# Kernel tuning notes

Hardware: AMD Instinct MI355X
Metric: run time of the kernel (lower is better)

## Reference

```python
import jax, jax.numpy as jnp
import numpy as np

T, B, E, H = 1024, 4, 1024, 16
Dh = E // H
NEG_INF = float('-inf')


def setup_inputs() -> dict:
    key = jax.random.key(0)
    k1, k2, k3, k4 = jax.random.split(key, 4)
    return {
        'fwd_x': jax.random.normal(k1, (T, B, E), jnp.float32),
        'bwd_x': jax.random.normal(k2, (T, B, E), jnp.float32),
        'in_proj_weight': jax.random.normal(k3, (3 * E, E), jnp.float32) * 0.02,
        'in_proj_bias': jnp.zeros((3 * E,), jnp.float32),
        'out_w': jax.random.normal(k4, (E, E), jnp.float32) * 0.02,
        'out_b': jnp.zeros((E,), jnp.float32),
    }


def reference(fwd_x, bwd_x, in_proj_weight, in_proj_bias, out_w, out_b):
    t, b, e = fwd_x.shape
    s = 2 * t
    dtype = fwd_x.dtype
    zeros = jnp.zeros((1, b, e), dtype)
    # padded_fwd_x[0:t] -> [0, fwd_x[:-1]]; padded_bwd_x[1:t+1] -> [bwd_x[1:], 0]
    q_in = jnp.concatenate([zeros, fwd_x[:-1]], 0) + jnp.concatenate([bwd_x[1:], zeros], 0)
    kv = jnp.concatenate([fwd_x, bwd_x], 0)  # [s, b, e]

    wq, wk, wv = in_proj_weight[:e], in_proj_weight[e:2 * e], in_proj_weight[2 * e:]
    bq, bk, bv = in_proj_bias[:e], in_proj_bias[e:2 * e], in_proj_bias[2 * e:]
    q = (q_in @ wq.T + bq).reshape(t, b, H, Dh)
    k = (kv @ wk.T + bk).reshape(s, b, H, Dh)
    v = (kv @ wv.T + bv).reshape(s, b, H, Dh)

    # NOTE: original module never applies self.scaling in forward -- keep unscaled.
    attn_weights = jnp.einsum('tbhd,sbhd->bhts', q, k)  # [b, H, t, s]

    # mask_curr_state=True: allowed keys are j < i (fwd half) or j > i + t (bwd half)
    i = jnp.arange(t)[:, None]
    j = jnp.arange(s)[None, :]
    allowed = (j >= i + t + 1) | (j <= i - 1)
    mask_bias = jnp.where(allowed, 0.0, NEG_INF).astype(dtype)
    attn_weights = attn_weights + mask_bias[None, None]

    probs = jax.nn.softmax(attn_weights.astype(jnp.float32), axis=-1).astype(dtype)

    attn = jnp.einsum('bhts,sbhd->tbhd', probs, v).reshape(t, b, e)
    attn = attn @ out_w.T + out_b
    avg_weights = probs.mean(axis=1)  # [b, t, s]
    return attn, avg_weights
```

## Files before the change

### kernel.cpp

```cpp
#include <hip/hip_runtime.h>

typedef unsigned short u16;
typedef __attribute__((ext_vector_type(8))) short short8;
typedef __attribute__((ext_vector_type(4))) float f32x4;

#define SM_SHIFT2 34.6246800f
#if defined(__has_builtin)
#if __has_builtin(__builtin_amdgcn_exp2f)
#define EXP2(x) __builtin_amdgcn_exp2f(x)
#else
#define EXP2(x) __expf((x) * 0.6931471805599453f)
#endif
#else
#define EXP2(x) __expf((x) * 0.6931471805599453f)
#endif

__device__ __forceinline__ u16 f2b(float f) {
  unsigned u = __float_as_uint(f);
  unsigned r = (u + 0x7FFFu + ((u >> 16) & 1u)) >> 16;
  return (u16)r;
}

__device__ __forceinline__ void gload16(const u16* g, u16* l) {
  __builtin_amdgcn_global_load_lds((const __attribute__((address_space(1))) void*)g,
                                   (__attribute__((address_space(3))) void*)l, 16, 0, 0);
}

__device__ __forceinline__ void cast4(const float* __restrict__ src,
                                      u16* __restrict__ dst, int gid) {
  float4 v = *(const float4*)(src + (gid << 2));
  ushort4 o; o.x = f2b(v.x); o.y = f2b(v.y); o.z = f2b(v.z); o.w = f2b(v.w);
  *(ushort4*)(dst + (gid << 2)) = o;
}

__global__ __launch_bounds__(256) void prep_all(const float* __restrict__ fwd,
                                                const float* __restrict__ bwd,
                                                const float* __restrict__ w_in,
                                                const float* __restrict__ w_out,
                                                u16* __restrict__ qin,
                                                u16* __restrict__ kvf,
                                                u16* __restrict__ kvb,
                                                u16* __restrict__ wbf,
                                                u16* __restrict__ wobf,
                                                float* __restrict__ out_avg) {
  const int blk = blockIdx.x, tid = threadIdx.x;
  if (blk < 4096) {
    int gid = blk * 256 + tid;
    int n = gid >> 8;
    int e4 = (gid & 255) << 2;
    int t = n >> 2, b = n & 3;
    float4 acc = make_float4(0.f, 0.f, 0.f, 0.f);
    if (t > 0) {
      float4 v = *(const float4*)(fwd + (((t - 1) * 4 + b) << 10) + e4);
      acc.x += v.x; acc.y += v.y; acc.z += v.z; acc.w += v.w;
    }
    if (t < 1023) {
      float4 v = *(const float4*)(bwd + (((t + 1) * 4 + b) << 10) + e4);
      acc.x += v.x; acc.y += v.y; acc.z += v.z; acc.w += v.w;
    }
    ushort4 o; o.x = f2b(acc.x); o.y = f2b(acc.y); o.z = f2b(acc.z); o.w = f2b(acc.w);
    *(ushort4*)(qin + (n << 10) + e4) = o;
  } else if (blk < 8192) {
    cast4(fwd, kvf, (blk - 4096) * 256 + tid);
  } else if (blk < 12288) {
    cast4(bwd, kvb, (blk - 8192) * 256 + tid);
  } else if (blk < 15360) {
    cast4(w_in, wbf, (blk - 12288) * 256 + tid);
  } else if (blk < 16384) {
    cast4(w_out, wobf, (blk - 15360) * 256 + tid);
  } else {
    int z = blk - 16384;
    int mi = z % 15, bt2 = z / 15;
    int tb2 = bt2 & 15, b2 = bt2 >> 4;
    int s0z = (tb2 + 1 + mi) << 6, t0z = tb2 << 6;
    float* ob = out_avg + (size_t)b2 * 2097152 + (size_t)t0z * 2048 + s0z;
    float4 zz = make_float4(0.f, 0.f, 0.f, 0.f);
#pragma unroll
    for (int it = 0; it < 4; ++it) {
      int idx = it * 256 + tid;
      int rr = idx >> 4, c4 = (idx & 15) << 2;
      *(float4*)&ob[rr * 2048 + c4] = zz;
    }
  }
}

__global__ __launch_bounds__(512, 2) void gemm_kv256(const u16* __restrict__ A,
                                                     const u16* __restrict__ W,
                                                     const float* __restrict__ bias,
                                                     u16* __restrict__ outK,
                                                     u16* __restrict__ outVt) {
  __shared__ u16 SH[65536];
  const int x = blockIdx.x & 7, local = blockIdx.x >> 3;
  const int mt = x * 4 + (local & 3);
  const int nt = local >> 2;
  const int m0 = mt << 8, n0 = nt << 8;
  const int tid = threadIdx.x;
  const int lane = tid & 63, wid = tid >> 6;
  const int wm = (wid >> 2) << 7;
  const int wn = (wid & 3) << 6;
  const int lr = lane & 15, lg = lane >> 4;
  const int co0 = ((lg ^ (lr & 7)) << 3);
  const int co1 = (((4 + lg) ^ (lr & 7)) << 3);
  const int rl = tid >> 3, ch = tid & 7;
  const int ssw = ((ch ^ (rl & 7)) << 3);
  const int arow = (rl & 31) + ((rl >> 5) << 7);
  f32x4 acc[8][4] = {};
  auto At = [&](int buf) { return SH + buf * 16384; };
  auto Wt = [&](int buf) { return SH + 32768 + buf * 16384; };
  auto stage_w2 = [&](int buf, int k0, int h) {
    int wr0 = (h << 7) + rl;
    gload16(&W[(size_t)(n0 + wr0) * 1024 + k0 + ssw], &Wt(buf)[wr0 * 64 + ch * 8]);
    int wr1 = wr0 + 64;
    gload16(&W[(size_t)(n0 + wr1) * 1024 + k0 + ssw], &Wt(buf)[wr1 * 64 + ch * 8]);
  };
  auto stage_a2 = [&](int buf, int k0, int h) {
    int ar0 = (h << 6) + arow;
    gload16(&A[(size_t)(m0 + ar0) * 1024 + k0 + ssw], &At(buf)[ar0 * 64 + ch * 8]);
    int ar1 = ar0 + 32;
    gload16(&A[(size_t)(m0 + ar1) * 1024 + k0 + ssw], &At(buf)[ar1 * 64 + ch * 8]);
  };
  stage_w2(0, 0, 0); stage_w2(0, 0, 1); stage_a2(0, 0, 0); stage_a2(0, 0, 1);
  short8 wf[4][2];
  for (int t = 0; t < 16; ++t) {
    const int cur = t & 1;
    const u16* a = At(cur);
    const u16* w = Wt(cur);
    const bool pf = (t < 15);
    const int nk0 = (t + 1) << 6;
#pragma unroll
    for (int q = 0; q < 4; ++q) {
      if (q == 0)      asm volatile("s_waitcnt vmcnt(3)" ::: "memory");
      else if (q == 1) { if (pf) asm volatile("s_waitcnt vmcnt(4)" ::: "memory");
                         else    asm volatile("s_waitcnt vmcnt(2)" ::: "memory"); }
      else if (q == 2) { if (pf) asm volatile("s_waitcnt vmcnt(5)" ::: "memory");
                         else    asm volatile("s_waitcnt vmcnt(1)" ::: "memory"); }
      else             { if (pf) asm volatile("s_waitcnt vmcnt(6)" ::: "memory");
                         else    asm volatile("s_waitcnt vmcnt(0)" ::: "memory"); }
      __builtin_amdgcn_s_barrier();
      if (pf) {
        if (q == 0) stage_w2(cur ^ 1, nk0, 0);
        else if (q == 1) stage_w2(cur ^ 1, nk0, 1);
        else if (q == 2) stage_a2(cur ^ 1, nk0, 0);
        else stage_a2(cur ^ 1, nk0, 1);
      }
      if (q == 0) {
#pragma unroll
        for (int j = 0; j < 4; ++j) {
          int wrow = (wn + j * 16 + lr) * 64;
          wf[j][0] = *(const short8*)&w[wrow + co0];
          wf[j][1] = *(const short8*)&w[wrow + co1];
        }
      }
      short8 af[2][2];
#pragma unroll
      for (int di = 0; di < 2; ++di) {
        int row = (wm + (2 * q + di) * 16 + lr) * 64;
        af[di][0] = *(const short8*)&a[row + co0];
        af[di][1] = *(const short8*)&a[row + co1];
      }
      __builtin_amdgcn_s_setprio(1);
#pragma unroll
      for (int dk = 0; dk < 2; ++dk)
#pragma unroll
        for (int di = 0; di < 2; ++di)
#pragma unroll
          for (int j = 0; j < 4; ++j)
            acc[2 * q + di][j] =
                __builtin_amdgcn_mfma_f32_16x16x32_bf16(af[di][dk], wf[j][dk],
                                                        acc[2 * q + di][j], 0, 0, 0);
      __builtin_amdgcn_s_setprio(0);
    }
  }
  __syncthreads();
  u16* C = SH;
  const bool isK = (n0 < 1024);
  if (isK) {
#pragma unroll
    for (int i = 0; i < 8; i++) {
#pragma unroll
      for (int j = 0; j < 4; j++) {
        int n = wn + j * 16 + lr;
        float bv = bias[n0 + n];
        int np = n ^ (lg << 4);
#pragma unroll
        for (int r = 0; r < 4; r++) {
          int m = wm + i * 16 + lg * 4 + r;
          C[m * 256 + np] = f2b(acc[i][j][r] + bv);
        }
      }
    }
    __syncthreads();
    const int hbase = n0 >> 6;
    const int ts0 = m0 >> 2;
    const int ts = tid >> 3, c8d = tid & 7;
#pragma unroll
    for (int k = 0; k < 16; ++k) {
      int tb = k >> 2, hh = k & 3;
      int m = ts * 4 + tb;
      int c8 = (hh * 8 + c8d) ^ ((ts & 3) << 1);
      uint4 val = *(const uint4*)&C[m * 256 + c8 * 8];
      size_t off = ((size_t)(tb * 16 + hbase + hh) * 2048 + ts0 + ts) * 64 + c8d * 8;
      *(uint4*)&outK[off] = val;
    }
  } else {
#pragma unroll
    for (int i = 0; i < 8; i++) {
#pragma unroll
      for (int j = 0; j < 4; j++) {
        int n = wn + j * 16 + lr;
        float bv = bias[n0 + n];
        int key = ((n & 7) ^ ((n >> 3) & 7)) << 3;
#pragma unroll
        for (int r = 0; r < 4; r++) {
          int u = (wm >> 2) + i * 4 + lg + (r << 6);
          C[n * 256 + (u ^ key)] = f2b(acc[i][j][r] + bv);
        }
      }
    }
    __syncthreads();
    const int dg0 = n0 - 1024;
    const int ts0 = m0 >> 2;
    const int nn = tid >> 3, tsg = tid & 7;
#pragma unroll
    for (int k = 0; k < 16; ++k) {
      int tb = k >> 2, nc = k & 3;
      int n = nc * 64 + nn;
      int key = ((n & 7) ^ ((n >> 3) & 7)) << 3;
      int chunk = ((tb << 6) + tsg * 8) ^ key;
      uint4 val = *(const uint4*)&C[n * 256 + chunk];
      int d = dg0 + n, h = d >> 6, dl = d & 63;
      size_t off = ((size_t)((tb * 16 + h) * 64 + dl)) * 2048 + ts0 + tsg * 8;
      *(uint4*)&outVt[off] = val;
    }
  }
}

template <int MODE, int MTX>
__global__ __launch_bounds__(256) void gemm_bt(const u16* __restrict__ A,
                                               const u16* __restrict__ W,
                                               const float* __restrict__ bias,
                                               void* __restrict__ outp) {
  __shared__ u16 At[2][128 * 64];
  __shared__ u16 Wt[2][128 * 64];
  const int x = blockIdx.x & 7, local = blockIdx.x >> 3;
  const int mt = x * MTX + (local % MTX);
  const int nt = local / MTX;
  const int m0 = mt << 7, n0 = nt << 7;
  const int tid = threadIdx.x;
  const int lane = tid & 63, wid = tid >> 6;
  const int wm = (wid >> 1) << 6, wn = (wid & 1) << 6;
  const int lr = lane & 15, lg = lane >> 4;
  const int srow = lane >> 3, scol = (lane & 7) << 3;
  const int swc = ((lane & 7) ^ srow) << 3;
  f32x4 acc[4][4] = {};
  auto stage = [&](int buf, int k0) {
#pragma unroll
    for (int it = 0; it < 4; it++) {
      int row = (it * 4 + wid) * 8 + srow;
      gload16(&A[(m0 + row) * 1024 + k0 + swc], &At[buf][row * 64 + scol]);
      gload16(&W[(n0 + row) * 1024 + k0 + swc], &Wt[buf][row * 64 + scol]);
    }
  };
  auto compute = [&](int buf) {
#pragma unroll
    for (int kk = 0; kk < 64; kk += 32) {
      short8 af[4], bf[4];
#pragma unroll
      for (int i = 0; i < 4; i++) {
        int co = (((kk >> 3) + lg) ^ (lr & 7)) << 3;
        af[i] = *(const short8*)&At[buf][(wm + i * 16 + lr) * 64 + co];
        bf[i] = *(const short8*)&Wt[buf][(wn + i * 16 + lr) * 64 + co];
      }
#pragma unroll
      for (int i = 0; i < 4; i++)
#pragma unroll
        for (int j = 0; j < 4; j++)
          acc[i][j] = __builtin_amdgcn_mfma_f32_16x16x32_bf16(af[i], bf[j], acc[i][j], 0, 0, 0);
    }
  };
  stage(0, 0);
  __syncthreads();
  for (int step = 0; step < 16; ++step) {
    const int cur = step & 1;
    if (step < 15) stage(cur ^ 1, (step + 1) << 6);
    compute(cur);
    __syncthreads();
  }
#pragma unroll
  for (int i = 0; i < 4; i++) {
#pragma unroll
    for (int j = 0; j < 4; j++) {
      int n = n0 + wn + j * 16 + lr;
      float bv = bias[n];
#pragma unroll
      for (int r = 0; r < 4; r++) {
        int m = m0 + wm + i * 16 + lg * 4 + r;
        float v = acc[i][j][r] + bv;
        if (MODE == 3) {
          ((float*)outp)[m * 1024 + n] = v;
        } else {
          v *= 1.44269504f;
          int tb = m & 3, ts = m >> 2, hh = n >> 6, d = n & 63;
          ((u16*)outp)[((tb * 16 + hh) * 1024 + ts) * 64 + d] = f2b(v);
        }
      }
    }
  }
}

__global__ __launch_bounds__(256) void attn_fwd(const u16* __restrict__ qb,
                                                const u16* __restrict__ kb,
                                                const u16* __restrict__ vtb,
                                                u16* __restrict__ attn_bf,
                                                float* __restrict__ st_il) {
  __shared__ u16 Kt[64 * 64];
  __shared__ u16 Vt[64 * 64];
  __shared__ u16 Pt[4][16 * 72];
  const int g = blockIdx.x;
  const int L = ((g & 7) << 7) | (g >> 3);
  const int t0 = (L & 15) << 6;
  const int h = (L >> 4) & 15;
  const int b = L >> 8;
  const int tid = threadIdx.x, lane = tid & 63, w = tid >> 6;
  const int lr = lane & 15, lg = lane >> 4;
  const int bh = b * 16 + h;
  const int sw0 = ((lg ^ (lr & 7)) << 3);
  const int sw1 = sw0 ^ 32;
  const u16* qrow = qb + ((bh << 10) + t0 + (w << 4) + lr) * 64;
  short8 qf0 = *(const short8*)&qrow[lg * 8];
  short8 qf1 = *(const short8*)&qrow[32 + lg * 8];
  const u16* kbase = kb + (size_t)(bh << 11) * 64;
  const u16* vbase = vtb + (size_t)(bh << 6) * 2048;
  f32x4 acc[4] = {};
  f32x4 accl = {};
  const int n1 = (t0 >> 6) + 1;
  const int grow = lane >> 3, gcol = (lane & 7) << 3;
  short8 ones;
#pragma unroll
  for (int j = 0; j < 8; ++j) ones[j] = (short)0x3F80;
  for (int ti = 0; ti < 17; ++ti) {
    const int s0 = (ti < n1) ? (ti << 6) : (t0 + 1024 + ((ti - n1) << 6));
    __syncthreads();
#pragma unroll
    for (int it = 0; it < 2; ++it) {
      int row = (it * 4 + w) * 8 + grow;
      int swc = (((lane & 7) ^ (row & 7)) << 3);
      gload16(&kbase[(size_t)(s0 + row) * 64 + swc], &Kt[row * 64 + gcol]);
      gload16(&vbase[(size_t)row * 2048 + s0 + swc], &Vt[row * 64 + gcol]);
    }
    __syncthreads();
    float pv[4][4];
    const bool maskt = (ti == n1 - 1) || (ti == n1);
    if (maskt) {
#pragma unroll
      for (int c = 0; c < 4; c++) {
        f32x4 sc = {};
        short8 kf0 = *(const short8*)&Kt[(c * 16 + lr) * 64 + sw0];
        short8 kf1 = *(const short8*)&Kt[(c * 16 + lr) * 64 + sw1];
        sc = __builtin_amdgcn_mfma_f32_16x16x32_bf16(qf0, kf0, sc, 0, 0, 0);
        sc = __builtin_amdgcn_mfma_f32_16x16x32_bf16(qf1, kf1, sc, 0, 0, 0);
        int j = s0 + c * 16 + lr;
#pragma unroll
        for (int r = 0; r < 4; r++) {
          int i = t0 + (w << 4) + lg * 4 + r;
          float e = EXP2(sc[r] - SM_SHIFT2);
          pv[c][r] = ((j < i) || (j > i + 1024)) ? e : 0.f;
        }
      }
    } else {
#pragma unroll
      for (int c = 0; c < 4; c++) {
        f32x4 sc = {};
        short8 kf0 = *(const short8*)&Kt[(c * 16 + lr) * 64 + sw0];
        short8 kf1 = *(const short8*)&Kt[(c * 16 + lr) * 64 + sw1];
        sc = __builtin_amdgcn_mfma_f32_16x16x32_bf16(qf0, kf0, sc, 0, 0, 0);
        sc = __builtin_amdgcn_mfma_f32_16x16x32_bf16(qf1, kf1, sc, 0, 0, 0);
#pragma unroll
        for (int r = 0; r < 4; r++)
          pv[c][r] = EXP2(sc[r] - SM_SHIFT2);
      }
    }
#pragma unroll
    for (int c = 0; c < 4; c++)
#pragma unroll
      for (int r = 0; r < 4; r++)
        Pt[w][(lg * 4 + r) * 72 + c * 16 + lr] = f2b(pv[c][r]);
    short8 pf0 = *(const short8*)&Pt[w][lr * 72 + lg * 8];
    short8 pf1 = *(const short8*)&Pt[w][lr * 72 + 32 + lg * 8];
    accl = __builtin_amdgcn_mfma_f32_16x16x32_bf16(pf0, ones, accl, 0, 0, 0);
    accl = __builtin_amdgcn_mfma_f32_16x16x32_bf16(pf1, ones, accl, 0, 0, 0);
#pragma unroll
    for (int dd = 0; dd < 4; dd++) {
      short8 vf0 = *(const short8*)&Vt[(dd * 16 + lr) * 64 + sw0];
      short8 vf1 = *(const short8*)&Vt[(dd * 16 + lr) * 64 + sw1];
      acc[dd] = __builtin_amdgcn_mfma_f32_16x16x32_bf16(pf0, vf0, acc[dd], 0, 0, 0);
      acc[dd] = __builtin_amdgcn_mfma_f32_16x16x32_bf16(pf1, vf1, acc[dd], 0, 0, 0);
    }
  }
  float inv[4];
#pragma unroll
  for (int r = 0; r < 4; r++) inv[r] = 1.f / accl[r];
  const int trow = t0 + (w << 4) + lg * 4;
#pragma unroll
  for (int dd = 0; dd < 4; dd++)
#pragma unroll
    for (int r = 0; r < 4; r++)
      attn_bf[((trow + r) * 4 + b) * 1024 + h * 64 + dd * 16 + lr] = f2b(acc[dd][r] * inv[r]);
#pragma unroll
  for (int r = 0; r < 4; r++)
    if (lr == r)
      st_il[(bh << 10) + trow + r] = inv[r];
}

__global__ __launch_bounds__(256) void attn_avg(const u16* __restrict__ qb,
                                                const u16* __restrict__ kb,
                                                const float* __restrict__ st_il,
                                                float* __restrict__ avg) {
  __shared__ u16 Kt[2][64 * 64];
  __shared__ float Si[16][64];
  const int g = blockIdx.x;
  const int L = (g & 7) * 136 + (g >> 3);
  const int l = L % 17;
  const int bt = L / 17;
  const int tb = bt & 15, b = bt >> 4;
  const int sb = (l <= tb) ? l : l + 15;
  const int s0 = sb << 6, t0 = tb << 6;
  const bool maskblk = (l == tb) || (l == tb + 1);
  const int tid = threadIdx.x, lane = tid & 63, w = tid >> 6;
  const int lr = lane & 15, lg = lane >> 4;
  const int trow = t0 + (w << 4) + lg * 4;
  float* obase = avg + (size_t)b * 2097152;
  for (int i = tid; i < 1024; i += 256) {
    int hh = i >> 6, tt = i & 63;
    Si[hh][tt] = st_il[(((b << 4) + hh) << 10) + t0 + tt];
  }
  const int sw0 = ((lg ^ (lr & 7)) << 3);
  const int sw1 = sw0 ^ 32;
  const int grow = lane >> 3, gcol = (lane & 7) << 3;
  const int srr = (w << 4) + lg * 4;
  auto stage = [&](int buf, int hh) {
    const u16* kb_h = kb + ((size_t)(((b << 4) + hh) << 11) + s0) * 64;
#pragma unroll
    for (int it = 0; it < 2; ++it) {
      int row = it * 32 + w * 8 + grow;
      int swc = (((lane & 7) ^ grow) << 3);
      gload16(&kb_h[(size_t)row * 64 + swc], &Kt[buf][row * 64 + gcol]);
    }
  };
  stage(0, 0);
  __syncthreads();
  float accv[4][4] = {};
  for (int h = 0; h < 16; h++) {
    const int cur = h & 1;
    if (h < 15) stage(cur ^ 1, h + 1);
    const int bh = (b << 4) + h;
    const u16* qrow = qb + ((bh << 10) + t0 + (w << 4) + lr) * 64;
    short8 qf0 = *(const short8*)&qrow[lg * 8];
    short8 qf1 = *(const short8*)&qrow[32 + lg * 8];
    float ih[4];
#pragma unroll
    for (int r = 0; r < 4; r++) ih[r] = Si[h][srr + r];
    if (maskblk) {
#pragma unroll
      for (int c = 0; c < 4; c++) {
        f32x4 sc = {};
        short8 kf0 = *(const short8*)&Kt[cur][(c * 16 + lr) * 64 + sw0];
        short8 kf1 = *(const short8*)&Kt[cur][(c * 16 + lr) * 64 + sw1];
        sc = __builtin_amdgcn_mfma_f32_16x16x32_bf16(qf0, kf0, sc, 0, 0, 0);
        sc = __builtin_amdgcn_mfma_f32_16x16x32_bf16(qf1, kf1, sc, 0, 0, 0);
        int j = s0 + c * 16 + lr;
#pragma unroll
        for (int r = 0; r < 4; r++) {
          int i = t0 + (w << 4) + lg * 4 + r;
          if ((j < i) || (j > i + 1024))
            accv[c][r] += EXP2(sc[r] - SM_SHIFT2) * ih[r];
        }
      }
    } else {
#pragma unroll
      for (int c = 0; c < 4; c++) {
        f32x4 sc = {};
        short8 kf0 = *(const short8*)&Kt[cur][(c * 16 + lr) * 64 + sw0];
        short8 kf1 = *(const short8*)&Kt[cur][(c * 16 + lr) * 64 + sw1];
        sc = __builtin_amdgcn_mfma_f32_16x16x32_bf16(qf0, kf0, sc, 0, 0, 0);
        sc = __builtin_amdgcn_mfma_f32_16x16x32_bf16(qf1, kf1, sc, 0, 0, 0);
#pragma unroll
        for (int r = 0; r < 4; r++)
          accv[c][r] += EXP2(sc[r] - SM_SHIFT2) * ih[r];
      }
    }
    __syncthreads();
  }
#pragma unroll
  for (int c = 0; c < 4; c++)
#pragma unroll
    for (int r = 0; r < 4; r++)
      obase[(trow + r) * 2048 + s0 + c * 16 + lr] = accv[c][r] * 0.0625f;
}

extern "C" void kernel_launch(void* const* d_in, const int* in_sizes, int n_in,
                              void* d_out, int out_size, void* d_ws, size_t ws_size,
                              hipStream_t stream) {
  const float* fwd   = (const float*)d_in[0];
  const float* bwd   = (const float*)d_in[1];
  const float* w_in  = (const float*)d_in[2];
  const float* b_in  = (const float*)d_in[3];
  const float* w_out = (const float*)d_in[4];
  const float* b_out = (const float*)d_in[5];

  char* ws = (char*)d_ws;
  u16*  q_in_bf = (u16*)(ws);
  u16*  kv_bf   = (u16*)(ws + 8388608);
  u16*  w_bf    = (u16*)(ws + 25165824);
  u16*  wo_bf   = (u16*)(ws + 31457280);
  u16*  q_bf    = (u16*)(ws + 33554432);
  u16*  k_bf    = (u16*)(ws + 41943040);
  u16*  vt_bf   = (u16*)(ws + 58720256);
  u16*  attn_bf = (u16*)(ws + 75497472);
  float* st_il  = (float*)(ws + 83886080);

  float* out_attn = (float*)d_out;
  float* out_avg  = (float*)d_out + 4194304;

  prep_all<<<17344, 256, 0, stream>>>(fwd, bwd, w_in, w_out, q_in_bf, kv_bf,
                                      kv_bf + 4194304, w_bf, wo_bf, out_avg);

  gemm_bt<0, 4><<<256, 256, 0, stream>>>(q_in_bf, w_bf, b_in, (void*)q_bf);
  gemm_kv256<<<256, 512, 0, stream>>>(kv_bf, w_bf + 1048576, b_in + 1024,
                                      k_bf, vt_bf);

  attn_fwd<<<1024, 256, 0, stream>>>(q_bf, k_bf, vt_bf, attn_bf, st_il);

  gemm_bt<3, 4><<<256, 256, 0, stream>>>(attn_bf, wo_bf, b_out,
                                         (void*)out_attn);

  attn_avg<<<1088, 256, 0, stream>>>(q_bf, k_bf, st_il, out_avg);
}
```

Before: 168.2 us.

## Merge Q projection into KV GEMM launch and fuse output GEMM with avg kernel

The Q projection now runs as 64 extra 256x256 tiles inside the KV projection kernel, with the log2e scale folded into its epilogue, so the standalone 128-tile Q GEMM launch goes away. The output projection GEMM and the attention-average kernel become one launch that dispatches on block index, letting the two independent tail stages share the GPU. This removes two launches and their tail gaps. In exchange, the fused out-projection path drops double buffering and syncs twice per k-step, and blocks of mixed shape may balance poorly.

Result: slower. 172.5 us (+2.5%).

```diff
diff --git a/kernel.cpp b/kernel.cpp
--- a/kernel.cpp
+++ b/kernel.cpp
@@ -84,16 +84,33 @@
   }
 }
 
-__global__ __launch_bounds__(512, 2) void gemm_kv256(const u16* __restrict__ A,
-                                                     const u16* __restrict__ W,
-                                                     const float* __restrict__ bias,
-                                                     u16* __restrict__ outK,
-                                                     u16* __restrict__ outVt) {
+__global__ __launch_bounds__(512, 2) void proj_qkv(const u16* __restrict__ kvA,
+                                                   const u16* __restrict__ Wkv,
+                                                   const float* __restrict__ bkv,
+                                                   const u16* __restrict__ qA,
+                                                   const u16* __restrict__ Wq,
+                                                   const float* __restrict__ bq,
+                                                   u16* __restrict__ outK,
+                                                   u16* __restrict__ outVt,
+                                                   u16* __restrict__ outQ) {
   __shared__ u16 SH[65536];
-  const int x = blockIdx.x & 7, local = blockIdx.x >> 3;
-  const int mt = x * 4 + (local & 3);
-  const int nt = local >> 2;
-  const int m0 = mt << 8, n0 = nt << 8;
+  const int bid = blockIdx.x;
+  const u16* A; const u16* W; const float* bias;
+  int m0, n0, path;
+  if (bid < 256) {
+    const int x = bid & 7, local = bid >> 3;
+    m0 = (x * 4 + (local & 3)) << 8;
+    n0 = (local >> 2) << 8;
+    A = kvA; W = Wkv; bias = bkv;
+    path = (n0 < 1024) ? 0 : 1;
+  } else {
+    const int l2 = bid - 256;
+    const int x = l2 & 7, loc = l2 >> 3;
+    m0 = ((x << 1) + (loc & 1)) << 8;
+    n0 = (loc >> 1) << 8;
+    A = qA; W = Wq; bias = bq;
+    path = 2;
+  }
   const int tid = threadIdx.x;
   const int lane = tid & 63, wid = tid >> 6;
   const int wm = (wid >> 2) << 7;
@@ -173,36 +190,7 @@
   }
   __syncthreads();
   u16* C = SH;
-  const bool isK = (n0 < 1024);
-  if (isK) {
-#pragma unroll
-    for (int i = 0; i < 8; i++) {
-#pragma unroll
-      for (int j = 0; j < 4; j++) {
-        int n = wn + j * 16 + lr;
-        float bv = bias[n0 + n];
-        int np = n ^ (lg << 4);
-#pragma unroll
-        for (int r = 0; r < 4; r++) {
-          int m = wm + i * 16 + lg * 4 + r;
-          C[m * 256 + np] = f2b(acc[i][j][r] + bv);
-        }
-      }
-    }
-    __syncthreads();
-    const int hbase = n0 >> 6;
-    const int ts0 = m0 >> 2;
-    const int ts = tid >> 3, c8d = tid & 7;
-#pragma unroll
-    for (int k = 0; k < 16; ++k) {
-      int tb = k >> 2, hh = k & 3;
-      int m = ts * 4 + tb;
-      int c8 = (hh * 8 + c8d) ^ ((ts & 3) << 1);
-      uint4 val = *(const uint4*)&C[m * 256 + c8 * 8];
-      size_t off = ((size_t)(tb * 16 + hbase + hh) * 2048 + ts0 + ts) * 64 + c8d * 8;
-      *(uint4*)&outK[off] = val;
-    }
-  } else {
+  if (path == 1) {
 #pragma unroll
     for (int i = 0; i < 8; i++) {
 #pragma unroll
@@ -232,78 +220,36 @@
       size_t off = ((size_t)((tb * 16 + h) * 64 + dl)) * 2048 + ts0 + tsg * 8;
       *(uint4*)&outVt[off] = val;
     }
-  }
-}
-
-template <int MODE, int MTX>
-__global__ __launch_bounds__(256) void gemm_bt(const u16* __restrict__ A,
-                                               const u16* __restrict__ W,
-                                               const float* __restrict__ bias,
-                                               void* __restrict__ outp) {
-  __shared__ u16 At[2][128 * 64];
-  __shared__ u16 Wt[2][128 * 64];
-  const int x = blockIdx.x & 7, local = blockIdx.x >> 3;
-  const int mt = x * MTX + (local % MTX);
-  const int nt = local / MTX;
-  const int m0 = mt << 7, n0 = nt << 7;
-  const int tid = threadIdx.x;
-  const int lane = tid & 63, wid = tid >> 6;
-  const int wm = (wid >> 1) << 6, wn = (wid & 1) << 6;
-  const int lr = lane & 15, lg = lane >> 4;
-  const int srow = lane >> 3, scol = (lane & 7) << 3;
-  const int swc = ((lane & 7) ^ srow) << 3;
-  f32x4 acc[4][4] = {};
-  auto stage = [&](int buf, int k0) {
-#pragma unroll
-    for (int it = 0; it < 4; it++) {
-      int row = (it * 4 + wid) * 8 + srow;
-      gload16(&A[(m0 + row) * 1024 + k0 + swc], &At[buf][row * 64 + scol]);
-      gload16(&W[(n0 + row) * 1024 + k0 + swc], &Wt[buf][row * 64 + scol]);
-    }
-  };
-  auto compute = [&](int buf) {
-#pragma unroll
-    for (int kk = 0; kk < 64; kk += 32) {
-      short8 af[4], bf[4];
-#pragma unroll
-      for (int i = 0; i < 4; i++) {
-        int co = (((kk >> 3) + lg) ^ (lr & 7)) << 3;
-        af[i] = *(const short8*)&At[buf][(wm + i * 16 + lr) * 64 + co];
-        bf[i] = *(const short8*)&Wt[buf][(wn + i * 16 + lr) * 64 + co];
-      }
-#pragma unroll
-      for (int i = 0; i < 4; i++)
-#pragma unroll
-        for (int j = 0; j < 4; j++)
-          acc[i][j] = __builtin_amdgcn_mfma_f32_16x16x32_bf16(af[i], bf[j], acc[i][j], 0, 0, 0);
-    }
-  };
-  stage(0, 0);
-  __syncthreads();
-  for (int step = 0; step < 16; ++step) {
-    const int cur = step & 1;
-    if (step < 15) stage(cur ^ 1, (step + 1) << 6);
-    compute(cur);
+  } else {
+    const float scl = (path == 2) ? 1.44269504f : 1.0f;
+#pragma unroll
+    for (int i = 0; i < 8; i++) {
+#pragma unroll
+      for (int j = 0; j < 4; j++) {
+        int n = wn + j * 16 + lr;
+        float bv = bias[n0 + n];
+        int np = n ^ (lg << 4);
+#pragma unroll
+        for (int r = 0; r < 4; r++) {
+          int m = wm + i * 16 + lg * 4 + r;
+          C[m * 256 + np] = f2b((acc[i][j][r] + bv) * scl);
+        }
+      }
+    }
     __syncthreads();
-  }
-#pragma unroll
-  for (int i = 0; i < 4; i++) {
-#pragma unroll
-    for (int j = 0; j < 4; j++) {
-      int n = n0 + wn + j * 16 + lr;
-      float bv = bias[n];
-#pragma unroll
-      for (int r = 0; r < 4; r++) {
-        int m = m0 + wm + i * 16 + lg * 4 + r;
-        float v = acc[i][j][r] + bv;
-        if (MODE == 3) {
-          ((float*)outp)[m * 1024 + n] = v;
-        } else {
-          v *= 1.44269504f;
-          int tb = m & 3, ts = m >> 2, hh = n >> 6, d = n & 63;
-          ((u16*)outp)[((tb * 16 + hh) * 1024 + ts) * 64 + d] = f2b(v);
-        }
-      }
+    u16* ob = (path == 0) ? outK : outQ;
+    const int SS = (path == 0) ? 2048 : 1024;
+    const int hbase = n0 >> 6;
+    const int ts0 = m0 >> 2;
+    const int ts = tid >> 3, c8d = tid & 7;
+#pragma unroll
+    for (int k = 0; k < 16; ++k) {
+      int tb = k >> 2, hh = k & 3;
+      int m = ts * 4 + tb;
+      int c8 = (hh * 8 + c8d) ^ ((ts & 3) << 1);
+      uint4 val = *(const uint4*)&C[m * 256 + c8 * 8];
+      size_t off = ((size_t)(tb * 16 + hbase + hh) * SS + ts0 + ts) * 64 + c8d * 8;
+      *(uint4*)&ob[off] = val;
     }
   }
 }
@@ -412,90 +358,149 @@
       st_il[(bh << 10) + trow + r] = inv[r];
 }
 
-__global__ __launch_bounds__(256) void attn_avg(const u16* __restrict__ qb,
-                                                const u16* __restrict__ kb,
-                                                const float* __restrict__ st_il,
-                                                float* __restrict__ avg) {
-  __shared__ u16 Kt[2][64 * 64];
-  __shared__ float Si[16][64];
-  const int g = blockIdx.x;
-  const int L = (g & 7) * 136 + (g >> 3);
-  const int l = L % 17;
-  const int bt = L / 17;
-  const int tb = bt & 15, b = bt >> 4;
-  const int sb = (l <= tb) ? l : l + 15;
-  const int s0 = sb << 6, t0 = tb << 6;
-  const bool maskblk = (l == tb) || (l == tb + 1);
-  const int tid = threadIdx.x, lane = tid & 63, w = tid >> 6;
+__global__ __launch_bounds__(256) void tail_mega(const u16* __restrict__ qb,
+                                                 const u16* __restrict__ kb,
+                                                 const float* __restrict__ st_il,
+                                                 float* __restrict__ avg,
+                                                 const u16* __restrict__ attA,
+                                                 const u16* __restrict__ wo,
+                                                 const float* __restrict__ bo,
+                                                 float* __restrict__ out_attn) {
+  __shared__ __align__(16) u16 SM[16384];
+  const int bid = blockIdx.x, tid = threadIdx.x;
+  const int lane = tid & 63, w = tid >> 6;
   const int lr = lane & 15, lg = lane >> 4;
-  const int trow = t0 + (w << 4) + lg * 4;
-  float* obase = avg + (size_t)b * 2097152;
-  for (int i = tid; i < 1024; i += 256) {
-    int hh = i >> 6, tt = i & 63;
-    Si[hh][tt] = st_il[(((b << 4) + hh) << 10) + t0 + tt];
+  if (bid < 1088) {
+    u16* KtF = SM;
+    float* Si = (float*)(SM + 8192);
+    const int L = (bid & 7) * 136 + (bid >> 3);
+    const int l = L % 17;
+    const int bt = L / 17;
+    const int tb = bt & 15, b = bt >> 4;
+    const int sb = (l <= tb) ? l : l + 15;
+    const int s0 = sb << 6, t0 = tb << 6;
+    const bool maskblk = (l == tb) || (l == tb + 1);
+    const int trow = t0 + (w << 4) + lg * 4;
+    float* obase = avg + (size_t)b * 2097152;
+    for (int i = tid; i < 1024; i += 256) {
+      int hh = i >> 6, tt = i & 63;
+      Si[hh * 64 + tt] = st_il[(((b << 4) + hh) << 10) + t0 + tt];
+    }
+    const int sw0 = ((lg ^ (lr & 7)) << 3);
+    const int sw1 = sw0 ^ 32;
+    const int grow = lane >> 3, gcol = (lane & 7) << 3;
+    const int srr = (w << 4) + lg * 4;
+    auto stage = [&](int buf, int hh) {
+      const u16* kb_h = kb + ((size_t)(((b << 4) + hh) << 11) + s0) * 64;
+#pragma unroll
+      for (int it = 0; it < 2; ++it) {
+        int row = it * 32 + w * 8 + grow;
+        int swc = (((lane & 7) ^ grow) << 3);
+        gload16(&kb_h[(size_t)row * 64 + swc], &KtF[buf * 4096 + row * 64 + gcol]);
+      }
+    };
+    stage(0, 0);
+    __syncthreads();
+    float accv[4][4] = {};
+    for (int h = 0; h < 16; h++) {
+      const int cur = h & 1;
+      if (h < 15) stage(cur ^ 1, h + 1);
+      const int bh = (b << 4) + h;
+      const u16* qrow = qb + ((bh << 10) + t0 + (w << 4) + lr) * 64;
+      short8 qf0 = *(const short8*)&qrow[lg * 8];
+      short8 qf1 = *(const short8*)&qrow[32 + lg * 8];
+      float ih[4];
+#pragma unroll
+      for (int r = 0; r < 4; r++) ih[r] = Si[h * 64 + srr + r];
+      const u16* Kc = KtF + cur * 4096;
+      if (maskblk) {
+#pragma unroll
+        for (int c = 0; c < 4; c++) {
+          f32x4 sc = {};
+          short8 kf0 = *(const short8*)&Kc[(c * 16 + lr) * 64 + sw0];
+          short8 kf1 = *(const short8*)&Kc[(c * 16 + lr) * 64 + sw1];
+          sc = __builtin_amdgcn_mfma_f32_16x16x32_bf16(qf0, kf0, sc, 0, 0, 0);
+          sc = __builtin_amdgcn_mfma_f32_16x16x32_bf16(qf1, kf1, sc, 0, 0, 0);
+          int j = s0 + c * 16 + lr;
+#pragma unroll
+          for (int r = 0; r < 4; r++) {
+            int i = t0 + (w << 4) + lg * 4 + r;
+            if ((j < i) || (j > i + 1024))
+              accv[c][r] += EXP2(sc[r] - SM_SHIFT2) * ih[r];
+          }
+        }
+      } else {
+#pragma unroll
+        for (int c = 0; c < 4; c++) {
+          f32x4 sc = {};
+          short8 kf0 = *(const short8*)&Kc[(c * 16 + lr) * 64 + sw0];
+          short8 kf1 = *(const short8*)&Kc[(c * 16 + lr) * 64 + sw1];
+          sc = __builtin_amdgcn_mfma_f32_16x16x32_bf16(qf0, kf0, sc, 0, 0, 0);
+          sc = __builtin_amdgcn_mfma_f32_16x16x32_bf16(qf1, kf1, sc, 0, 0, 0);
+#pragma unroll
+          for (int r = 0; r < 4; r++)
+            accv[c][r] += EXP2(sc[r] - SM_SHIFT2) * ih[r];
+        }
+      }
+      __syncthreads();
+    }
+#pragma unroll
+    for (int c = 0; c < 4; c++)
+#pragma unroll
+      for (int r = 0; r < 4; r++)
+        obase[(trow + r) * 2048 + s0 + c * 16 + lr] = accv[c][r] * 0.0625f;
+  } else {
+    u16* At = SM;
+    u16* Wt = SM + 8192;
+    const int b2 = bid - 1088;
+    const int x = b2 & 7, local = b2 >> 3;
+    const int mt = x * 4 + (local & 3);
+    const int nt = local >> 2;
+    const int m0 = mt << 7, n0 = nt << 7;
+    const int wid = w;
+    const int wm = (wid >> 1) << 6, wn = (wid & 1) << 6;
+    const int srow = lane >> 3, scol = (lane & 7) << 3;
+    const int swc = ((lane & 7) ^ srow) << 3;
+    f32x4 acc[4][4] = {};
+    for (int step = 0; step < 16; ++step) {
+      __syncthreads();
+#pragma unroll
+      for (int it = 0; it < 4; it++) {
+        int row = (it * 4 + wid) * 8 + srow;
+        gload16(&attA[(m0 + row) * 1024 + (step << 6) + swc], &At[row * 64 + scol]);
+        gload16(&wo[(n0 + row) * 1024 + (step << 6) + swc], &Wt[row * 64 + scol]);
+      }
+      __syncthreads();
+#pragma unroll
+      for (int kk = 0; kk < 64; kk += 32) {
+        short8 af[4], bf[4];
+#pragma unroll
+        for (int i = 0; i < 4; i++) {
+          int co = (((kk >> 3) + lg) ^ (lr & 7)) << 3;
+          af[i] = *(const short8*)&At[(wm + i * 16 + lr) * 64 + co];
+          bf[i] = *(const short8*)&Wt[(wn + i * 16 + lr) * 64 + co];
+        }
+#pragma unroll
+        for (int i = 0; i < 4; i++)
+#pragma unroll
+          for (int j = 0; j < 4; j++)
+            acc[i][j] = __builtin_amdgcn_mfma_f32_16x16x32_bf16(af[i], bf[j], acc[i][j], 0, 0, 0);
+      }
+    }
+#pragma unroll
+    for (int i = 0; i < 4; i++) {
+#pragma unroll
+      for (int j = 0; j < 4; j++) {
+        int n = n0 + wn + j * 16 + lr;
+        float bv = bo[n];
+#pragma unroll
+        for (int r = 0; r < 4; r++) {
+          int m = m0 + wm + i * 16 + lg * 4 + r;
+          out_attn[m * 1024 + n] = acc[i][j][r] + bv;
+        }
+      }
+    }
   }
-  const int sw0 = ((lg ^ (lr & 7)) << 3);
-  const int sw1 = sw0 ^ 32;
-  const int grow = lane >> 3, gcol = (lane & 7) << 3;
-  const int srr = (w << 4) + lg * 4;
-  auto stage = [&](int buf, int hh) {
-    const u16* kb_h = kb + ((size_t)(((b << 4) + hh) << 11) + s0) * 64;
-#pragma unroll
-    for (int it = 0; it < 2; ++it) {
-      int row = it * 32 + w * 8 + grow;
-      int swc = (((lane & 7) ^ grow) << 3);
-      gload16(&kb_h[(size_t)row * 64 + swc], &Kt[buf][row * 64 + gcol]);
-    }
-  };
-  stage(0, 0);
-  __syncthreads();
-  float accv[4][4] = {};
-  for (int h = 0; h < 16; h++) {
-    const int cur = h & 1;
-    if (h < 15) stage(cur ^ 1, h + 1);
-    const int bh = (b << 4) + h;
-    const u16* qrow = qb + ((bh << 10) + t0 + (w << 4) + lr) * 64;
-    short8 qf0 = *(const short8*)&qrow[lg * 8];
-    short8 qf1 = *(const short8*)&qrow[32 + lg * 8];
-    float ih[4];
-#pragma unroll
-    for (int r = 0; r < 4; r++) ih[r] = Si[h][srr + r];
-    if (maskblk) {
-#pragma unroll
-      for (int c = 0; c < 4; c++) {
-        f32x4 sc = {};
-        short8 kf0 = *(const short8*)&Kt[cur][(c * 16 + lr) * 64 + sw0];
-        short8 kf1 = *(const short8*)&Kt[cur][(c * 16 + lr) * 64 + sw1];
-        sc = __builtin_amdgcn_mfma_f32_16x16x32_bf16(qf0, kf0, sc, 0, 0, 0);
-        sc = __builtin_amdgcn_mfma_f32_16x16x32_bf16(qf1, kf1, sc, 0, 0, 0);
-        int j = s0 + c * 16 + lr;
-#pragma unroll
-        for (int r = 0; r < 4; r++) {
-          int i = t0 + (w << 4) + lg * 4 + r;
-          if ((j < i) || (j > i + 1024))
-            accv[c][r] += EXP2(sc[r] - SM_SHIFT2) * ih[r];
-        }
-      }
-    } else {
-#pragma unroll
-      for (int c = 0; c < 4; c++) {
-        f32x4 sc = {};
-        short8 kf0 = *(const short8*)&Kt[cur][(c * 16 + lr) * 64 + sw0];
-        short8 kf1 = *(const short8*)&Kt[cur][(c * 16 + lr) * 64 + sw1];
-        sc = __builtin_amdgcn_mfma_f32_16x16x32_bf16(qf0, kf0, sc, 0, 0, 0);
-        sc = __builtin_amdgcn_mfma_f32_16x16x32_bf16(qf1, kf1, sc, 0, 0, 0);
-#pragma unroll
-        for (int r = 0; r < 4; r++)
-          accv[c][r] += EXP2(sc[r] - SM_SHIFT2) * ih[r];
-      }
-    }
-    __syncthreads();
-  }
-#pragma unroll
-  for (int c = 0; c < 4; c++)
-#pragma unroll
-    for (int r = 0; r < 4; r++)
-      obase[(trow + r) * 2048 + s0 + c * 16 + lr] = accv[c][r] * 0.0625f;
 }
 
 extern "C" void kernel_launch(void* const* d_in, const int* in_sizes, int n_in,
@@ -525,14 +530,12 @@
   prep_all<<<17344, 256, 0, stream>>>(fwd, bwd, w_in, w_out, q_in_bf, kv_bf,
                                       kv_bf + 4194304, w_bf, wo_bf, out_avg);
 
-  gemm_bt<0, 4><<<256, 256, 0, stream>>>(q_in_bf, w_bf, b_in, (void*)q_bf);
-  gemm_kv256<<<256, 512, 0, stream>>>(kv_bf, w_bf + 1048576, b_in + 1024,
-                                      k_bf, vt_bf);
+  proj_qkv<<<320, 512, 0, stream>>>(kv_bf, w_bf + 1048576, b_in + 1024,
+                                    q_in_bf, w_bf, b_in,
+                                    k_bf, vt_bf, q_bf);
 
   attn_fwd<<<1024, 256, 0, stream>>>(q_bf, k_bf, vt_bf, attn_bf, st_il);
 
-  gemm_bt<3, 4><<<256, 256, 0, stream>>>(attn_bf, wo_bf, b_out,
-                                         (void*)out_attn);
-
-  attn_avg<<<1088, 256, 0, stream>>>(q_bf, k_bf, st_il, out_avg);
-}
+  tail_mega<<<1344, 256, 0, stream>>>(q_bf, k_bf, st_il, out_avg,
+                                      attn_bf, wo_bf, b_out, out_attn);
+}
```

## Fuse output projection GEMM and attention-average kernel into one launch

Applied to the files above, without the earlier changes.

Merges the output-projection GEMM and the head-averaged probability kernel into a single heterogeneous kernel. Block IDs are split into groups of 21: 17 blocks compute avg-weights tiles and 4 compute 128x128 GEMM tiles, so the two independent workloads run concurrently and share the GPU. This removes one launch and the tail/serialization gap between the two kernels. The cost is a shared LDS buffer sized for the larger role, which may reduce occupancy, and a GEMM path that is no longer the tuned gemm_bt template.

Result: slower. 173.7 us (+3.2%).

```diff
diff --git a/kernel.cpp b/kernel.cpp
--- a/kernel.cpp
+++ b/kernel.cpp
@@ -412,90 +412,150 @@
       st_il[(bh << 10) + trow + r] = inv[r];
 }
 
-__global__ __launch_bounds__(256) void attn_avg(const u16* __restrict__ qb,
-                                                const u16* __restrict__ kb,
-                                                const float* __restrict__ st_il,
-                                                float* __restrict__ avg) {
-  __shared__ u16 Kt[2][64 * 64];
-  __shared__ float Si[16][64];
-  const int g = blockIdx.x;
-  const int L = (g & 7) * 136 + (g >> 3);
-  const int l = L % 17;
-  const int bt = L / 17;
-  const int tb = bt & 15, b = bt >> 4;
-  const int sb = (l <= tb) ? l : l + 15;
-  const int s0 = sb << 6, t0 = tb << 6;
-  const bool maskblk = (l == tb) || (l == tb + 1);
-  const int tid = threadIdx.x, lane = tid & 63, w = tid >> 6;
+__global__ __launch_bounds__(256) void tail_mega(const u16* __restrict__ qb,
+                                                 const u16* __restrict__ kb,
+                                                 const float* __restrict__ st_il,
+                                                 float* __restrict__ avg,
+                                                 const u16* __restrict__ attA,
+                                                 const u16* __restrict__ wo,
+                                                 const float* __restrict__ bo,
+                                                 float* __restrict__ out_attn) {
+  __shared__ __align__(16) u16 SM[16384];
+  const int bid = blockIdx.x, tid = threadIdx.x;
+  const int lane = tid & 63, w = tid >> 6;
   const int lr = lane & 15, lg = lane >> 4;
-  const int trow = t0 + (w << 4) + lg * 4;
-  float* obase = avg + (size_t)b * 2097152;
-  for (int i = tid; i < 1024; i += 256) {
-    int hh = i >> 6, tt = i & 63;
-    Si[hh][tt] = st_il[(((b << 4) + hh) << 10) + t0 + tt];
-  }
-  const int sw0 = ((lg ^ (lr & 7)) << 3);
-  const int sw1 = sw0 ^ 32;
-  const int grow = lane >> 3, gcol = (lane & 7) << 3;
-  const int srr = (w << 4) + lg * 4;
-  auto stage = [&](int buf, int hh) {
-    const u16* kb_h = kb + ((size_t)(((b << 4) + hh) << 11) + s0) * 64;
-#pragma unroll
-    for (int it = 0; it < 2; ++it) {
-      int row = it * 32 + w * 8 + grow;
-      int swc = (((lane & 7) ^ grow) << 3);
-      gload16(&kb_h[(size_t)row * 64 + swc], &Kt[buf][row * 64 + gcol]);
-    }
-  };
-  stage(0, 0);
-  __syncthreads();
-  float accv[4][4] = {};
-  for (int h = 0; h < 16; h++) {
-    const int cur = h & 1;
-    if (h < 15) stage(cur ^ 1, h + 1);
-    const int bh = (b << 4) + h;
-    const u16* qrow = qb + ((bh << 10) + t0 + (w << 4) + lr) * 64;
-    short8 qf0 = *(const short8*)&qrow[lg * 8];
-    short8 qf1 = *(const short8*)&qrow[32 + lg * 8];
-    float ih[4];
-#pragma unroll
-    for (int r = 0; r < 4; r++) ih[r] = Si[h][srr + r];
-    if (maskblk) {
-#pragma unroll
-      for (int c = 0; c < 4; c++) {
-        f32x4 sc = {};
-        short8 kf0 = *(const short8*)&Kt[cur][(c * 16 + lr) * 64 + sw0];
-        short8 kf1 = *(const short8*)&Kt[cur][(c * 16 + lr) * 64 + sw1];
-        sc = __builtin_amdgcn_mfma_f32_16x16x32_bf16(qf0, kf0, sc, 0, 0, 0);
-        sc = __builtin_amdgcn_mfma_f32_16x16x32_bf16(qf1, kf1, sc, 0, 0, 0);
-        int j = s0 + c * 16 + lr;
+  const int grp = bid / 21, off = bid % 21;
+  if (off < 17) {
+    u16* KtF = SM;
+    float* Si = (float*)(SM + 8192);
+    const int aidx = grp * 17 + off;
+    const int l = aidx % 17;
+    const int bt = aidx / 17;
+    const int tb = bt & 15, b = bt >> 4;
+    const int sb = (l <= tb) ? l : l + 15;
+    const int s0 = sb << 6, t0 = tb << 6;
+    const bool maskblk = (l == tb) || (l == tb + 1);
+    const int trow = t0 + (w << 4) + lg * 4;
+    float* obase = avg + (size_t)b * 2097152;
+    for (int i = tid; i < 1024; i += 256) {
+      int hh = i >> 6, tt = i & 63;
+      Si[hh * 64 + tt] = st_il[(((b << 4) + hh) << 10) + t0 + tt];
+    }
+    const int sw0 = ((lg ^ (lr & 7)) << 3);
+    const int sw1 = sw0 ^ 32;
+    const int grow = lane >> 3, gcol = (lane & 7) << 3;
+    const int srr = (w << 4) + lg * 4;
+    auto stage = [&](int buf, int hh) {
+      const u16* kb_h = kb + ((size_t)(((b << 4) + hh) << 11) + s0) * 64;
+#pragma unroll
+      for (int it = 0; it < 2; ++it) {
+        int row = it * 32 + w * 8 + grow;
+        int swc = (((lane & 7) ^ grow) << 3);
+        gload16(&kb_h[(size_t)row * 64 + swc], &KtF[buf * 4096 + row * 64 + gcol]);
+      }
+    };
+    stage(0, 0);
+    __syncthreads();
+    float accv[4][4] = {};
+    for (int h = 0; h < 16; h++) {
+      const int cur = h & 1;
+      if (h < 15) stage(cur ^ 1, h + 1);
+      const int bh = (b << 4) + h;
+      const u16* qrow = qb + ((bh << 10) + t0 + (w << 4) + lr) * 64;
+      short8 qf0 = *(const short8*)&qrow[lg * 8];
+      short8 qf1 = *(const short8*)&qrow[32 + lg * 8];
+      float ih[4];
+#pragma unroll
+      for (int r = 0; r < 4; r++) ih[r] = Si[h * 64 + srr + r];
+      const u16* Kc = KtF + cur * 4096;
+      if (maskblk) {
+#pragma unroll
+        for (int c = 0; c < 4; c++) {
+          f32x4 sc = {};
+          short8 kf0 = *(const short8*)&Kc[(c * 16 + lr) * 64 + sw0];
+          short8 kf1 = *(const short8*)&Kc[(c * 16 + lr) * 64 + sw1];
+          sc = __builtin_amdgcn_mfma_f32_16x16x32_bf16(qf0, kf0, sc, 0, 0, 0);
+          sc = __builtin_amdgcn_mfma_f32_16x16x32_bf16(qf1, kf1, sc, 0, 0, 0);
+          int j = s0 + c * 16 + lr;
+#pragma unroll
+          for (int r = 0; r < 4; r++) {
+            int i = t0 + (w << 4) + lg * 4 + r;
+            if ((j < i) || (j > i + 1024))
+              accv[c][r] += EXP2(sc[r] - SM_SHIFT2) * ih[r];
+          }
+        }
+      } else {
+#pragma unroll
+        for (int c = 0; c < 4; c++) {
+          f32x4 sc = {};
+          short8 kf0 = *(const short8*)&Kc[(c * 16 + lr) * 64 + sw0];
+          short8 kf1 = *(const short8*)&Kc[(c * 16 + lr) * 64 + sw1];
+          sc = __builtin_amdgcn_mfma_f32_16x16x32_bf16(qf0, kf0, sc, 0, 0, 0);
+          sc = __builtin_amdgcn_mfma_f32_16x16x32_bf16(qf1, kf1, sc, 0, 0, 0);
+#pragma unroll
+          for (int r = 0; r < 4; r++)
+            accv[c][r] += EXP2(sc[r] - SM_SHIFT2) * ih[r];
+        }
+      }
+      __syncthreads();
+    }
+#pragma unroll
+    for (int c = 0; c < 4; c++)
+#pragma unroll
+      for (int r = 0; r < 4; r++)
+        obase[(trow + r) * 2048 + s0 + c * 16 + lr] = accv[c][r] * 0.0625f;
+  } else {
+    u16* At = SM;
+    u16* Wt = SM + 8192;
+    const int oidx = grp * 4 + (off - 17);
+    const int x = oidx & 7, local = oidx >> 3;
+    const int mt = x * 4 + (local & 3);
+    const int nt = local >> 2;
+    const int m0 = mt << 7, n0 = nt << 7;
+    const int wid = w;
+    const int wm = (wid >> 1) << 6, wn = (wid & 1) << 6;
+    const int srow = lane >> 3, scol = (lane & 7) << 3;
+    const int swc = ((lane & 7) ^ srow) << 3;
+    f32x4 acc[4][4] = {};
+    for (int step = 0; step < 16; ++step) {
+      __syncthreads();
+#pragma unroll
+      for (int it = 0; it < 4; it++) {
+        int row = (it * 4 + wid) * 8 + srow;
+        gload16(&attA[(m0 + row) * 1024 + (step << 6) + swc], &At[row * 64 + scol]);
+        gload16(&wo[(n0 + row) * 1024 + (step << 6) + swc], &Wt[row * 64 + scol]);
+      }
+      __syncthreads();
+#pragma unroll
+      for (int kk = 0; kk < 64; kk += 32) {
+        short8 af[4], bf[4];
+#pragma unroll
+        for (int i = 0; i < 4; i++) {
+          int co = (((kk >> 3) + lg) ^ (lr & 7)) << 3;
+          af[i] = *(const short8*)&At[(wm + i * 16 + lr) * 64 + co];
+          bf[i] = *(const short8*)&Wt[(wn + i * 16 + lr) * 64 + co];
+        }
+#pragma unroll
+        for (int i = 0; i < 4; i++)
+#pragma unroll
+          for (int j = 0; j < 4; j++)
+            acc[i][j] = __builtin_amdgcn_mfma_f32_16x16x32_bf16(af[i], bf[j], acc[i][j], 0, 0, 0);
+      }
+    }
+#pragma unroll
+    for (int i = 0; i < 4; i++) {
+#pragma unroll
+      for (int j = 0; j < 4; j++) {
+        int n = n0 + wn + j * 16 + lr;
+        float bv = bo[n];
 #pragma unroll
         for (int r = 0; r < 4; r++) {
-          int i = t0 + (w << 4) + lg * 4 + r;
-          if ((j < i) || (j > i + 1024))
-            accv[c][r] += EXP2(sc[r] - SM_SHIFT2) * ih[r];
-        }
-      }
-    } else {
-#pragma unroll
-      for (int c = 0; c < 4; c++) {
-        f32x4 sc = {};
-        short8 kf0 = *(const short8*)&Kt[cur][(c * 16 + lr) * 64 + sw0];
-        short8 kf1 = *(const short8*)&Kt[cur][(c * 16 + lr) * 64 + sw1];
-        sc = __builtin_amdgcn_mfma_f32_16x16x32_bf16(qf0, kf0, sc, 0, 0, 0);
-        sc = __builtin_amdgcn_mfma_f32_16x16x32_bf16(qf1, kf1, sc, 0, 0, 0);
-#pragma unroll
-        for (int r = 0; r < 4; r++)
-          accv[c][r] += EXP2(sc[r] - SM_SHIFT2) * ih[r];
-      }
-    }
-    __syncthreads();
-  }
-#pragma unroll
-  for (int c = 0; c < 4; c++)
-#pragma unroll
-    for (int r = 0; r < 4; r++)
-      obase[(trow + r) * 2048 + s0 + c * 16 + lr] = accv[c][r] * 0.0625f;
+          int m = m0 + wm + i * 16 + lg * 4 + r;
+          out_attn[m * 1024 + n] = acc[i][j][r] + bv;
+        }
+      }
+    }
+  }
 }
 
 extern "C" void kernel_launch(void* const* d_in, const int* in_sizes, int n_in,
@@ -531,8 +591,6 @@
 
   attn_fwd<<<1024, 256, 0, stream>>>(q_bf, k_bf, vt_bf, attn_bf, st_il);
 
-  gemm_bt<3, 4><<<256, 256, 0, stream>>>(attn_bf, wo_bf, b_out,
-                                         (void*)out_attn);
-
-  attn_avg<<<1088, 256, 0, stream>>>(q_bf, k_bf, st_il, out_avg);
-}
+  tail_mega<<<1344, 256, 0, stream>>>(q_bf, k_bf, st_il, out_avg,
+                                      attn_bf, wo_bf, b_out, out_attn);
+}
```
